# Kernel optimization log

Measured on AMD Instinct MI355X. Metric: run time of the kernel, lower is better.

Reference implementation:

```python
import jax, jax.numpy as jnp
import numpy as np

GAMMA = 5e-4
IN_DIM, HID = 512, 4096
N = HID  # batch must equal hidden_dim for classifier(gram) to type-check


def setup_inputs() -> dict:
    key = jax.random.key(0)
    ks = jax.random.split(key, 7)
    s = lambda fan_in: 1.0 / np.sqrt(fan_in)
    return {
        "x": jax.random.normal(ks[0], (N, IN_DIM), jnp.float32),
        "W1": jax.random.uniform(ks[1], (HID, IN_DIM), jnp.float32, -s(IN_DIM), s(IN_DIM)),
        "b1": jax.random.uniform(ks[2], (HID,), jnp.float32, -s(IN_DIM), s(IN_DIM)),
        "W2": jax.random.uniform(ks[3], (HID, HID), jnp.float32, -s(HID), s(HID)),
        "b2": jax.random.uniform(ks[4], (HID,), jnp.float32, -s(HID), s(HID)),
        "Wc": jax.random.uniform(ks[5], (1, HID), jnp.float32, -s(HID), s(HID)),
        "bc": jax.random.uniform(ks[6], (1,), jnp.float32, -s(HID), s(HID)),
    }


def reference(x, W1, b1, W2, b2, Wc, bc):
    h = jnp.tanh(x @ W1.T + b1)          # [N, HID]
    h = jnp.tanh(h @ W2.T + b2)          # [N, HID]
    # KernelLayer: support = h.detach() (first call), RBF gram via cdist+exp
    support = jax.lax.stop_gradient(h)   # [N, HID]
    sq = (jnp.sum(h * h, axis=1, keepdims=True)
          + jnp.sum(support * support, axis=1)[None, :]
          - 2.0 * (h @ support.T))       # [N, N] squared distances
    gram = jnp.exp(-GAMMA * sq)
    return gram @ Wc.T + bc              # [N, 1]
```

## Files before the change

kernel.cpp:

```cpp
#include <hip/hip_runtime.h>
#include <hip/hip_bf16.h>


#define NROWS 4096
#define HID   4096
#define INDIM 512
#define GAMMA_F 5e-4f

typedef float f32x4  __attribute__((ext_vector_type(4)));
typedef int   i32x4  __attribute__((ext_vector_type(4)));
typedef int   i32x8  __attribute__((ext_vector_type(8)));

#define BAR() asm volatile("s_barrier" ::: "memory")
#define SCALE1 0x7F7F7F7F

#define MFMA16(d, a, b) \
    d = __builtin_amdgcn_mfma_scale_f32_16x16x128_f8f6f4( \
        a, b, d, 0, 0, 0, SCALE1, 0, SCALE1)

__device__ __forceinline__ unsigned char f2e4m3(float x) {
  unsigned int u = __float_as_uint(x);
  unsigned char s = (unsigned char)((u >> 24) & 0x80u);
  float a = fabsf(x);
  if (a >= 448.f) return s | 0x7E;
  if (a < 0.015625f) {
    int q = (int)rintf(a * 512.f);
    return s | (unsigned char)q;
  }
  unsigned int ua = u & 0x7fffffffu;
  ua += 0x7FFFFu + ((ua >> 20) & 1u);
  int e = (int)(ua >> 23) - 127;
  unsigned int m = (ua >> 20) & 7u;
  return s | (unsigned char)(((e + 7) << 3) | m);
}

__global__ void prep(const float* __restrict__ x, const float* __restrict__ W1,
                     const float* __restrict__ W2, const float* __restrict__ bc,
                     unsigned char* __restrict__ xq, unsigned char* __restrict__ w1q,
                     unsigned char* __restrict__ w2q,
                     float* __restrict__ out, float* __restrict__ norms) {
  const int gi = blockIdx.x * blockDim.x + threadIdx.x;
  if (gi < NROWS) { out[gi] = bc[0]; norms[gi] = 0.f; }
  const int NX  = NROWS * INDIM / 8;
  const int NW2 = HID * HID / 8;
  const int total = 2 * NX + NW2;
  const int stride = gridDim.x * blockDim.x;
  for (int i = gi; i < total; i += stride) {
    const float* src; unsigned char* dst; float sc; int j;
    if (i < NX)          { src = x;  dst = xq;  sc = 16.f;  j = i; }
    else if (i < 2 * NX) { src = W1; dst = w1q; sc = 32.f;  j = i - NX; }
    else                 { src = W2; dst = w2q; sc = 128.f; j = i - 2 * NX; }
    float4 v0 = ((const float4*)src)[j * 2];
    float4 v1 = ((const float4*)src)[j * 2 + 1];
    unsigned int r0 = (unsigned int)f2e4m3(v0.x * sc)
                    | ((unsigned int)f2e4m3(v0.y * sc) << 8)
                    | ((unsigned int)f2e4m3(v0.z * sc) << 16)
                    | ((unsigned int)f2e4m3(v0.w * sc) << 24);
    unsigned int r1 = (unsigned int)f2e4m3(v1.x * sc)
                    | ((unsigned int)f2e4m3(v1.y * sc) << 8)
                    | ((unsigned int)f2e4m3(v1.z * sc) << 16)
                    | ((unsigned int)f2e4m3(v1.w * sc) << 24);
    uint2 o; o.x = r0; o.y = r1;
    ((uint2*)dst)[j] = o;
  }
}

__device__ __forceinline__ void gload16(const void* g, void* l) {
  __builtin_amdgcn_global_load_lds(
      (const __attribute__((address_space(1))) void*)g,
      (__attribute__((address_space(3))) void*)l, 16, 0, 0);
}

#define LDFRAG(dst, base0, off, RSTRIDE) do {                       \
    i32x4 lo_ = *(const i32x4*)((base0) + (off));                   \
    i32x4 hi_ = *(const i32x4*)((base0) + (RSTRIDE) + (off));       \
    dst = __builtin_shufflevector(lo_, hi_, 0, 1, 2, 3, 4, 5, 6, 7); } while (0)

template <int EPI>
__global__ __launch_bounds__(512, 2)
void gemm256_fp8(const unsigned char* __restrict__ A, const unsigned char* __restrict__ B,
                 int K, int N,
                 const float* __restrict__ bias, unsigned char* __restrict__ Hout,
                 float* __restrict__ norms_out) {
  __shared__ __align__(16) unsigned char As[2][2][256 * 64];
  __shared__ __align__(16) unsigned char Bs[2][2][256 * 64];

  const int tid  = threadIdx.x;
  const int lane = tid & 63;
  const int wave = tid >> 6;
  const int wr = wave >> 2, wc = wave & 3;
  const int fr = lane & 15, fq = lane >> 4;

  const int nwg = gridDim.x;
  const int cpx = nwg >> 3;
  const int bid = blockIdx.x;
  const int swzb = (bid & 7) * cpx + (bid >> 3);
  const int nbx = N >> 8;
  const int brow = (swzb / nbx) << 8;
  const int bcol = (swzb % nbx) << 8;

  const unsigned char* ap[4]; const unsigned char* bp[4]; int ldq[4];
#pragma unroll
  for (int q = 0; q < 4; ++q) {
    int idx = q * 512 + tid;
    int h   = idx >> 10;
    int row = (idx >> 2) & 255;
    int c   = idx & 3;
    int gcol = ((((c ^ ((row >> 1) & 3)) << 1) | h) << 4);
    ap[q] = A + (size_t)(brow + row) * K + gcol;
    bp[q] = B + (size_t)(bcol + row) * K + gcol;
    ldq[q] = (q * 512 + wave * 64) * 16;
  }
#define STAGE_A(p, tt) do { int kk = (tt) * 128;              \
    gload16(ap[0] + kk, &As[p][0][0] + ldq[0]);               \
    gload16(ap[1] + kk, &As[p][0][0] + ldq[1]);               \
    gload16(ap[2] + kk, &As[p][0][0] + ldq[2]);               \
    gload16(ap[3] + kk, &As[p][0][0] + ldq[3]); } while (0)
#define STAGE_B(p, tt) do { int kk = (tt) * 128;              \
    gload16(bp[0] + kk, &Bs[p][0][0] + ldq[0]);               \
    gload16(bp[1] + kk, &Bs[p][0][0] + ldq[1]);               \
    gload16(bp[2] + kk, &Bs[p][0][0] + ldq[2]);               \
    gload16(bp[3] + kk, &Bs[p][0][0] + ldq[3]); } while (0)

  int aoff[8], boff[4];
#pragma unroll
  for (int mi = 0; mi < 8; ++mi) {
    int row = wr * 128 + mi * 16 + fr;
    aoff[mi] = row * 64 + ((fq ^ ((row >> 1) & 3)) << 4);
  }
#pragma unroll
  for (int nj = 0; nj < 4; ++nj) {
    int row = wc * 64 + nj * 16 + fr;
    boff[nj] = row * 64 + ((fq ^ ((row >> 1) & 3)) << 4);
  }

  const int NT = K >> 7;

  STAGE_A(0, 0); STAGE_B(0, 0);
  STAGE_A(1, 1); STAGE_B(1, 1);
  asm volatile("s_waitcnt vmcnt(8)" ::: "memory");
  BAR();

  f32x4 acc[8][4] = {};
  i32x8 afr[4], bfr[4];

  for (int t = 0; t < NT; ++t) {
    const int p = t & 1;
    int t2 = t + 2; if (t2 >= NT) t2 = NT - 1;

#pragma unroll
    for (int mi = 0; mi < 4; ++mi) LDFRAG(afr[mi], &As[p][0][0], aoff[mi], 16384);
#pragma unroll
    for (int nj = 0; nj < 4; ++nj) LDFRAG(bfr[nj], &Bs[p][0][0], boff[nj], 16384);
    asm volatile("s_waitcnt lgkmcnt(0)" ::: "memory");
    BAR();
    STAGE_B(p, t2);
    __builtin_amdgcn_sched_barrier(0);
    __builtin_amdgcn_s_setprio(1);
#pragma unroll
    for (int mi = 0; mi < 4; ++mi)
#pragma unroll
      for (int nj = 0; nj < 4; ++nj) MFMA16(acc[mi][nj], afr[mi], bfr[nj]);
    __builtin_amdgcn_s_setprio(0);

#pragma unroll
    for (int mi = 0; mi < 4; ++mi) LDFRAG(afr[mi], &As[p][0][0], aoff[4 + mi], 16384);
    asm volatile("s_waitcnt lgkmcnt(0)" ::: "memory");
    BAR();
    STAGE_A(p, t2);
    __builtin_amdgcn_sched_barrier(0);
    __builtin_amdgcn_s_setprio(1);
#pragma unroll
    for (int mi = 0; mi < 4; ++mi)
#pragma unroll
      for (int nj = 0; nj < 4; ++nj) MFMA16(acc[4 + mi][nj], afr[mi], bfr[nj]);
    __builtin_amdgcn_s_setprio(0);
    asm volatile("s_waitcnt vmcnt(8)" ::: "memory");
    BAR();
  }
  asm volatile("s_waitcnt vmcnt(0)" ::: "memory");

  const float rescale = (EPI == 0) ? (1.f / 512.f) : (1.f / 1024.f);
  float bv[4];
#pragma unroll
  for (int nj = 0; nj < 4; ++nj) bv[nj] = bias[bcol + wc * 64 + nj * 16 + fr];
#pragma unroll
  for (int mi = 0; mi < 8; ++mi) {
    int row0 = brow + wr * 128 + mi * 16 + fq * 4;
#pragma unroll
    for (int rr = 0; rr < 4; ++rr) {
      float ns = 0.f;
#pragma unroll
      for (int nj = 0; nj < 4; ++nj) {
        int col = bcol + wc * 64 + nj * 16 + fr;
        float v = tanhf(acc[mi][nj][rr] * rescale + bv[nj]);
        Hout[(size_t)(row0 + rr) * N + col] = f2e4m3(8.f * v);
        if (EPI == 2) ns += v * v;
      }
      if (EPI == 2) {
        ns += __shfl_xor(ns, 1);
        ns += __shfl_xor(ns, 2);
        ns += __shfl_xor(ns, 4);
        ns += __shfl_xor(ns, 8);
        if (fr == 0) atomicAdd(&norms_out[row0 + rr], ns);
      }
    }
  }
#undef STAGE_A
#undef STAGE_B
}

__global__ __launch_bounds__(256, 2)
void gram_tri(const unsigned char* __restrict__ H, int K,
              const float* __restrict__ norms, const float* __restrict__ Wc,
              float* __restrict__ out) {
  __shared__ __align__(16) unsigned char As[2][128 * 64];
  __shared__ __align__(16) unsigned char Bs[2][128 * 64];

  const int tid  = threadIdx.x;
  const int lane = tid & 63;
  const int wave = tid >> 6;
  const int wr = wave >> 1, wc = wave & 1;
  const int fr = lane & 15, fq = lane >> 4;

  const int bid = blockIdx.x;
  const int swzb = (bid & 7) * 66 + (bid >> 3);
  int I = (int)((sqrtf(8.0f * (float)swzb + 1.0f) - 1.0f) * 0.5f);
  while ((I + 1) * (I + 2) / 2 <= swzb) ++I;
  while (I * (I + 1) / 2 > swzb) --I;
  const int J = swzb - I * (I + 1) / 2;
  const int brow = I << 7, bcol = J << 7;
  const bool diag = (I == J);

  const unsigned char* ap[4]; const unsigned char* bp[4]; int ldq[4];
#pragma unroll
  for (int q = 0; q < 4; ++q) {
    int idx = q * 256 + tid;
    int h   = idx >> 9;
    int row = (idx >> 2) & 127;
    int c   = idx & 3;
    int gcol = ((((c ^ ((row >> 1) & 3)) << 1) | h) << 4);
    ap[q] = H + (size_t)(brow + row) * K + gcol;
    bp[q] = H + (size_t)(bcol + row) * K + gcol;
    ldq[q] = (q * 256 + wave * 64) * 16;
  }

  int aoff[4], boff[4];
#pragma unroll
  for (int mi = 0; mi < 4; ++mi) {
    int row = wr * 64 + mi * 16 + fr;
    aoff[mi] = row * 64 + ((fq ^ ((row >> 1) & 3)) << 4);
  }
#pragma unroll
  for (int nj = 0; nj < 4; ++nj) {
    int row = wc * 64 + nj * 16 + fr;
    boff[nj] = row * 64 + ((fq ^ ((row >> 1) & 3)) << 4);
  }

  f32x4 acc[4][4] = {};

  for (int t = 0; t < (K >> 7); ++t) {
    __syncthreads();
    {
      int kk = t * 128;
      gload16(ap[0] + kk, &As[0][0] + ldq[0]);
      gload16(ap[1] + kk, &As[0][0] + ldq[1]);
      gload16(ap[2] + kk, &As[0][0] + ldq[2]);
      gload16(ap[3] + kk, &As[0][0] + ldq[3]);
      gload16(bp[0] + kk, &Bs[0][0] + ldq[0]);
      gload16(bp[1] + kk, &Bs[0][0] + ldq[1]);
      gload16(bp[2] + kk, &Bs[0][0] + ldq[2]);
      gload16(bp[3] + kk, &Bs[0][0] + ldq[3]);
    }
    __syncthreads();

    i32x8 af[4], bf[4];
#pragma unroll
    for (int mi = 0; mi < 4; ++mi) LDFRAG(af[mi], &As[0][0], aoff[mi], 8192);
#pragma unroll
    for (int nj = 0; nj < 4; ++nj) LDFRAG(bf[nj], &Bs[0][0], boff[nj], 8192);
#pragma unroll
    for (int mi = 0; mi < 4; ++mi)
#pragma unroll
      for (int nj = 0; nj < 4; ++nj)
        acc[mi][nj] = __builtin_amdgcn_mfma_scale_f32_16x16x128_f8f6f4(
            af[mi], bf[nj], acc[mi][nj], 0, 0, 0, SCALE1, 0, SCALE1);
  }

  float ncol[4], wcv[4];
#pragma unroll
  for (int nj = 0; nj < 4; ++nj) {
    int col = bcol + wc * 64 + nj * 16 + fr;
    ncol[nj] = norms[col];
    wcv[nj]  = Wc[col];
  }
  float colpart[4] = {0.f, 0.f, 0.f, 0.f};
#pragma unroll
  for (int mi = 0; mi < 4; ++mi) {
    int row0 = brow + wr * 64 + mi * 16 + fq * 4;
    float4 nr4  = *(const float4*)&norms[row0];
    float4 wcr4 = *(const float4*)&Wc[row0];
#pragma unroll
    for (int rr = 0; rr < 4; ++rr) {
      float nrow = (rr == 0) ? nr4.x : (rr == 1) ? nr4.y : (rr == 2) ? nr4.z : nr4.w;
      float wrow = (rr == 0) ? wcr4.x : (rr == 1) ? wcr4.y : (rr == 2) ? wcr4.z : wcr4.w;
      float rowpart = 0.f;
#pragma unroll
      for (int nj = 0; nj < 4; ++nj) {
        float sq = nrow + ncol[nj] - acc[mi][nj][rr] * 0.03125f;
        float e = __expf(-GAMMA_F * sq);
        rowpart += e * wcv[nj];
        colpart[nj] += e * wrow;
      }
      rowpart += __shfl_xor(rowpart, 1);
      rowpart += __shfl_xor(rowpart, 2);
      rowpart += __shfl_xor(rowpart, 4);
      rowpart += __shfl_xor(rowpart, 8);
      if (fr == 0) atomicAdd(&out[row0 + rr], rowpart);
    }
  }
  if (!diag) {
#pragma unroll
    for (int nj = 0; nj < 4; ++nj) {
      colpart[nj] += __shfl_xor(colpart[nj], 16);
      colpart[nj] += __shfl_xor(colpart[nj], 32);
      if (fq == 0) atomicAdd(&out[bcol + wc * 64 + nj * 16 + fr], colpart[nj]);
    }
  }
}

extern "C" void kernel_launch(void* const* d_in, const int* in_sizes, int n_in,
                              void* d_out, int out_size, void* d_ws, size_t ws_size,
                              hipStream_t stream) {
  const float* x  = (const float*)d_in[0];
  const float* W1 = (const float*)d_in[1];
  const float* b1 = (const float*)d_in[2];
  const float* W2 = (const float*)d_in[3];
  const float* b2 = (const float*)d_in[4];
  const float* Wc = (const float*)d_in[5];
  const float* bc = (const float*)d_in[6];
  float* out = (float*)d_out;

  char* ws = (char*)d_ws;
  unsigned char* xq  = (unsigned char*)ws; ws += (size_t)NROWS * INDIM;
  unsigned char* w1q = (unsigned char*)ws; ws += (size_t)HID * INDIM;
  unsigned char* w2q = (unsigned char*)ws; ws += (size_t)HID * HID;
  unsigned char* h1q = (unsigned char*)ws; ws += (size_t)NROWS * HID;
  unsigned char* h2q = (unsigned char*)ws; ws += (size_t)NROWS * HID;
  float* norms = (float*)ws;                ws += (size_t)NROWS * 4;

  prep<<<2048, 256, 0, stream>>>(x, W1, W2, bc, xq, w1q, w2q, out, norms);

  const int grid = (NROWS / 256) * (HID / 256);

  gemm256_fp8<0><<<grid, 512, 0, stream>>>(xq, w1q, INDIM, HID, b1, h1q, nullptr);
  gemm256_fp8<2><<<grid, 512, 0, stream>>>(h1q, w2q, HID, HID, b2, h2q, norms);
  gram_tri<<<528, 256, 0, stream>>>(h2q, HID, norms, Wc, out);
}
```

Measured before the change: 193.7 us.

## Replace 256-tile pipelined GEMM with simple 128-tile kernel; register-prefetch in gram

```diff
diff --git a/kernel.cpp b/kernel.cpp
--- a/kernel.cpp
+++ b/kernel.cpp
@@ -11,7 +11,6 @@
 typedef int   i32x4  __attribute__((ext_vector_type(4)));
 typedef int   i32x8  __attribute__((ext_vector_type(8)));
 
-#define BAR() asm volatile("s_barrier" ::: "memory")
 #define SCALE1 0x7F7F7F7F
 
 #define MFMA16(d, a, b) \
@@ -77,55 +76,45 @@
     dst = __builtin_shufflevector(lo_, hi_, 0, 1, 2, 3, 4, 5, 6, 7); } while (0)
 
 template <int EPI>
-__global__ __launch_bounds__(512, 2)
-void gemm256_fp8(const unsigned char* __restrict__ A, const unsigned char* __restrict__ B,
+__global__ __launch_bounds__(256, 4)
+void gemm128_fp8(const unsigned char* __restrict__ A, const unsigned char* __restrict__ B,
                  int K, int N,
                  const float* __restrict__ bias, unsigned char* __restrict__ Hout,
                  float* __restrict__ norms_out) {
-  __shared__ __align__(16) unsigned char As[2][2][256 * 64];
-  __shared__ __align__(16) unsigned char Bs[2][2][256 * 64];
+  __shared__ __align__(16) unsigned char As[2][128 * 64];
+  __shared__ __align__(16) unsigned char Bs[2][128 * 64];
 
   const int tid  = threadIdx.x;
   const int lane = tid & 63;
   const int wave = tid >> 6;
-  const int wr = wave >> 2, wc = wave & 3;
+  const int wr = wave >> 1, wc = wave & 1;
   const int fr = lane & 15, fq = lane >> 4;
 
   const int nwg = gridDim.x;
   const int cpx = nwg >> 3;
   const int bid = blockIdx.x;
   const int swzb = (bid & 7) * cpx + (bid >> 3);
-  const int nbx = N >> 8;
-  const int brow = (swzb / nbx) << 8;
-  const int bcol = (swzb % nbx) << 8;
+  const int nbx = N >> 7;
+  const int brow = (swzb / nbx) << 7;
+  const int bcol = (swzb % nbx) << 7;
 
   const unsigned char* ap[4]; const unsigned char* bp[4]; int ldq[4];
 #pragma unroll
   for (int q = 0; q < 4; ++q) {
-    int idx = q * 512 + tid;
-    int h   = idx >> 10;
-    int row = (idx >> 2) & 255;
+    int idx = q * 256 + tid;
+    int h   = idx >> 9;
+    int row = (idx >> 2) & 127;
     int c   = idx & 3;
     int gcol = ((((c ^ ((row >> 1) & 3)) << 1) | h) << 4);
     ap[q] = A + (size_t)(brow + row) * K + gcol;
     bp[q] = B + (size_t)(bcol + row) * K + gcol;
-    ldq[q] = (q * 512 + wave * 64) * 16;
-  }
-#define STAGE_A(p, tt) do { int kk = (tt) * 128;              \
-    gload16(ap[0] + kk, &As[p][0][0] + ldq[0]);               \
-    gload16(ap[1] + kk, &As[p][0][0] + ldq[1]);               \
-    gload16(ap[2] + kk, &As[p][0][0] + ldq[2]);               \
-    gload16(ap[3] + kk, &As[p][0][0] + ldq[3]); } while (0)
-#define STAGE_B(p, tt) do { int kk = (tt) * 128;              \
-    gload16(bp[0] + kk, &Bs[p][0][0] + ldq[0]);               \
-    gload16(bp[1] + kk, &Bs[p][0][0] + ldq[1]);               \
-    gload16(bp[2] + kk, &Bs[p][0][0] + ldq[2]);               \
-    gload16(bp[3] + kk, &Bs[p][0][0] + ldq[3]); } while (0)
-
-  int aoff[8], boff[4];
-#pragma unroll
-  for (int mi = 0; mi < 8; ++mi) {
-    int row = wr * 128 + mi * 16 + fr;
+    ldq[q] = (q * 256 + wave * 64) * 16;
+  }
+
+  int aoff[4], boff[4];
+#pragma unroll
+  for (int mi = 0; mi < 4; ++mi) {
+    int row = wr * 64 + mi * 16 + fr;
     aoff[mi] = row * 64 + ((fq ^ ((row >> 1) & 3)) << 4);
   }
 #pragma unroll
@@ -134,59 +123,41 @@
     boff[nj] = row * 64 + ((fq ^ ((row >> 1) & 3)) << 4);
   }
 
-  const int NT = K >> 7;
-
-  STAGE_A(0, 0); STAGE_B(0, 0);
-  STAGE_A(1, 1); STAGE_B(1, 1);
-  asm volatile("s_waitcnt vmcnt(8)" ::: "memory");
-  BAR();
-
-  f32x4 acc[8][4] = {};
-  i32x8 afr[4], bfr[4];
-
-  for (int t = 0; t < NT; ++t) {
-    const int p = t & 1;
-    int t2 = t + 2; if (t2 >= NT) t2 = NT - 1;
-
-#pragma unroll
-    for (int mi = 0; mi < 4; ++mi) LDFRAG(afr[mi], &As[p][0][0], aoff[mi], 16384);
-#pragma unroll
-    for (int nj = 0; nj < 4; ++nj) LDFRAG(bfr[nj], &Bs[p][0][0], boff[nj], 16384);
-    asm volatile("s_waitcnt lgkmcnt(0)" ::: "memory");
-    BAR();
-    STAGE_B(p, t2);
-    __builtin_amdgcn_sched_barrier(0);
-    __builtin_amdgcn_s_setprio(1);
+  f32x4 acc[4][4] = {};
+
+  for (int t = 0; t < (K >> 7); ++t) {
+    __syncthreads();
+    {
+      int kk = t * 128;
+      gload16(ap[0] + kk, &As[0][0] + ldq[0]);
+      gload16(ap[1] + kk, &As[0][0] + ldq[1]);
+      gload16(ap[2] + kk, &As[0][0] + ldq[2]);
+      gload16(ap[3] + kk, &As[0][0] + ldq[3]);
+      gload16(bp[0] + kk, &Bs[0][0] + ldq[0]);
+      gload16(bp[1] + kk, &Bs[0][0] + ldq[1]);
+      gload16(bp[2] + kk, &Bs[0][0] + ldq[2]);
+      gload16(bp[3] + kk, &Bs[0][0] + ldq[3]);
+    }
+    __syncthreads();
+
+    i32x8 af[4], bf[4];
+#pragma unroll
+    for (int mi = 0; mi < 4; ++mi) LDFRAG(af[mi], &As[0][0], aoff[mi], 8192);
+#pragma unroll
+    for (int nj = 0; nj < 4; ++nj) LDFRAG(bf[nj], &Bs[0][0], boff[nj], 8192);
 #pragma unroll
     for (int mi = 0; mi < 4; ++mi)
 #pragma unroll
-      for (int nj = 0; nj < 4; ++nj) MFMA16(acc[mi][nj], afr[mi], bfr[nj]);
-    __builtin_amdgcn_s_setprio(0);
-
-#pragma unroll
-    for (int mi = 0; mi < 4; ++mi) LDFRAG(afr[mi], &As[p][0][0], aoff[4 + mi], 16384);
-    asm volatile("s_waitcnt lgkmcnt(0)" ::: "memory");
-    BAR();
-    STAGE_A(p, t2);
-    __builtin_amdgcn_sched_barrier(0);
-    __builtin_amdgcn_s_setprio(1);
-#pragma unroll
-    for (int mi = 0; mi < 4; ++mi)
-#pragma unroll
-      for (int nj = 0; nj < 4; ++nj) MFMA16(acc[4 + mi][nj], afr[mi], bfr[nj]);
-    __builtin_amdgcn_s_setprio(0);
-    asm volatile("s_waitcnt vmcnt(8)" ::: "memory");
-    BAR();
-  }
-  asm volatile("s_waitcnt vmcnt(0)" ::: "memory");
+      for (int nj = 0; nj < 4; ++nj) MFMA16(acc[mi][nj], af[mi], bf[nj]);
+  }
 
   const float rescale = (EPI == 0) ? (1.f / 512.f) : (1.f / 1024.f);
   float bv[4];
 #pragma unroll
   for (int nj = 0; nj < 4; ++nj) bv[nj] = bias[bcol + wc * 64 + nj * 16 + fr];
 #pragma unroll
-  for (int mi = 0; mi < 8; ++mi) {
-    int row0 = brow + wr * 128 + mi * 16 + fq * 4;
+  for (int mi = 0; mi < 4; ++mi) {
+    int row0 = brow + wr * 64 + mi * 16 + fq * 4;
 #pragma unroll
     for (int rr = 0; rr < 4; ++rr) {
       float ns = 0.f;
@@ -206,8 +177,6 @@
       }
     }
   }
-#undef STAGE_A
-#undef STAGE_B
 }
 
 __global__ __launch_bounds__(256, 2)
@@ -232,7 +201,7 @@
   const int brow = I << 7, bcol = J << 7;
   const bool diag = (I == J);
 
-  const unsigned char* ap[4]; const unsigned char* bp[4]; int ldq[4];
+  const unsigned char* ap[4]; const unsigned char* bp[4]; int wq[4];
 #pragma unroll
   for (int q = 0; q < 4; ++q) {
     int idx = q * 256 + tid;
@@ -242,7 +211,7 @@
     int gcol = ((((c ^ ((row >> 1) & 3)) << 1) | h) << 4);
     ap[q] = H + (size_t)(brow + row) * K + gcol;
     bp[q] = H + (size_t)(bcol + row) * K + gcol;
-    ldq[q] = (q * 256 + wave * 64) * 16;
+    wq[q] = idx * 16;
   }
 
   int aoff[4], boff[4];
@@ -257,22 +226,29 @@
     boff[nj] = row * 64 + ((fq ^ ((row >> 1) & 3)) << 4);
   }
 
+  const int NT = K >> 7;
   f32x4 acc[4][4] = {};
-
-  for (int t = 0; t < (K >> 7); ++t) {
-    __syncthreads();
-    {
-      int kk = t * 128;
-      gload16(ap[0] + kk, &As[0][0] + ldq[0]);
-      gload16(ap[1] + kk, &As[0][0] + ldq[1]);
-      gload16(ap[2] + kk, &As[0][0] + ldq[2]);
-      gload16(ap[3] + kk, &As[0][0] + ldq[3]);
-      gload16(bp[0] + kk, &Bs[0][0] + ldq[0]);
-      gload16(bp[1] + kk, &Bs[0][0] + ldq[1]);
-      gload16(bp[2] + kk, &Bs[0][0] + ldq[2]);
-      gload16(bp[3] + kk, &Bs[0][0] + ldq[3]);
-    }
-    __syncthreads();
+  i32x4 rA[4], rB[4];
+
+#pragma unroll
+  for (int q = 0; q < 4; ++q) {
+    rA[q] = *(const i32x4*)(ap[q]);
+    rB[q] = *(const i32x4*)(bp[q]);
+  }
+#pragma unroll
+  for (int q = 0; q < 4; ++q) {
+    *(i32x4*)(&As[0][0] + wq[q]) = rA[q];
+    *(i32x4*)(&Bs[0][0] + wq[q]) = rB[q];
+  }
+  __syncthreads();
+
+  for (int t = 0; t < NT; ++t) {
+    int tn = t + 1; if (tn >= NT) tn = NT - 1;
+#pragma unroll
+    for (int q = 0; q < 4; ++q) {
+      rA[q] = *(const i32x4*)(ap[q] + tn * 128);
+      rB[q] = *(const i32x4*)(bp[q] + tn * 128);
+    }
 
     i32x8 af[4], bf[4];
 #pragma unroll
@@ -285,6 +261,14 @@
       for (int nj = 0; nj < 4; ++nj)
         acc[mi][nj] = __builtin_amdgcn_mfma_scale_f32_16x16x128_f8f6f4(
             af[mi], bf[nj], acc[mi][nj], 0, 0, 0, SCALE1, 0, SCALE1);
+
+    __syncthreads();
+#pragma unroll
+    for (int q = 0; q < 4; ++q) {
+      *(i32x4*)(&As[0][0] + wq[q]) = rA[q];
+      *(i32x4*)(&Bs[0][0] + wq[q]) = rB[q];
+    }
+    __syncthreads();
   }
 
   float ncol[4], wcv[4];
@@ -351,9 +335,9 @@
 
   prep<<<2048, 256, 0, stream>>>(x, W1, W2, bc, xq, w1q, w2q, out, norms);
 
-  const int grid = (NROWS / 256) * (HID / 256);
-
-  gemm256_fp8<0><<<grid, 512, 0, stream>>>(xq, w1q, INDIM, HID, b1, h1q, nullptr);
-  gemm256_fp8<2><<<grid, 512, 0, stream>>>(h1q, w2q, HID, HID, b2, h2q, norms);
+  const int grid = (NROWS / 128) * (HID / 128);
+
+  gemm128_fp8<0><<<grid, 256, 0, stream>>>(xq, w1q, INDIM, HID, b1, h1q, nullptr);
+  gemm128_fp8<2><<<grid, 256, 0, stream>>>(h1q, w2q, HID, HID, b2, h2q, norms);
   gram_tri<<<528, 256, 0, stream>>>(h2q, HID, norms, Wc, out);
 }
```

New measurement: 199.4 us. +2.9%, slower.
